# Optimization experiments

Hardware: AMD Instinct MI355X
Metric: run time of the kernel (lower is better)

Reference implementation:

```python
import math
import jax, jax.numpy as jnp
import numpy as np

B, S, D = 2, 2048, 1024
H = 16
R = 256
NC = 16
NE = 16
NK = 4096
KR = 256
TOPK = 8


def setup_inputs() -> dict:
    key = jax.random.key(0)
    ks = jax.random.split(key, 16)
    n = lambda k, shape, s: jax.random.normal(k, shape, jnp.float32) * s
    d = {}
    d['x'] = jax.random.normal(ks[0], (B, S, D), jnp.float32)
    d['importance'] = jax.random.uniform(ks[1], (B, S), jnp.float32)
    # global router weights (nn.Linear(d_model, n, bias=False) -> [n, d_model])
    d['Wc'] = n(ks[2], (NC, D), 0.02)
    d['WQ'] = n(ks[3], (NE, D), 0.02)
    d['WK'] = n(ks[4], (NE, D), 0.02)
    d['WV'] = n(ks[5], (NE, D), 0.02)
    d['Wm'] = n(ks[6], (NC, D), 0.02)
    # shared neuron pools (orthogonal init approximated by scaled gaussian)
    d['compress_neurons'] = n(ks[7], (NC, D, R), 1.0 / math.sqrt(D))
    d['expand_pool'] = n(ks[8], (NE, R, D), 1.0 / math.sqrt(R))
    d['knowledge_K'] = n(ks[9], (NK, KR), 0.02)
    d['knowledge_V'] = n(ks[10], (NK, D), 0.02)
    d['W_O'] = n(ks[11], (D, D), 1.0 / math.sqrt(D))
    d['g1'] = jnp.ones((D,), jnp.float32)
    d['b1'] = jnp.zeros((D,), jnp.float32)
    d['g2'] = jnp.ones((D,), jnp.float32)
    d['b2'] = jnp.zeros((D,), jnp.float32)
    return d


def _ln(x, g, b):
    mu = x.mean(-1, keepdims=True)
    v = ((x - mu) ** 2).mean(-1, keepdims=True)
    return (x - mu) * jax.lax.rsqrt(v + 1e-5) * g + b


def _route(nx, imp, W):
    # softmax over expert axis, importance-weighted pool over sequence, renormalize
    pref = jax.nn.softmax(nx @ W.T, axis=-1)          # [B,S,n]
    w = jnp.einsum('bs,bsn->bn', imp, pref)
    return w / (w.sum(-1, keepdims=True) + 1e-8)


def reference(x, importance, Wc, WQ, WK, WV, Wm, compress_neurons, expand_pool,
              knowledge_K, knowledge_V, W_O, g1, b1, g2, b2):
    Bx, Sx, Dm = x.shape
    dh = Dm // H
    # --- attention sub-block ---
    nx = _ln(x, g1, b1)
    cw = _route(nx, importance, Wc)
    qw = _route(nx, importance, WQ)
    kw = _route(nx, importance, WK)
    vw = _route(nx, importance, WV)
    sc = jnp.einsum('bn,ndr->bdr', cw, compress_neurons)   # per-batch compress [B,D,R]
    h = jnp.einsum('bsd,bdr->bsr', nx, sc)                 # [B,S,R]

    def expand(w):
        e = jnp.einsum('bn,nrd->brd', w, expand_pool)      # [B,R,D]
        return jnp.einsum('bsr,brd->bsd', h, e)            # [B,S,D]

    Q = expand(qw).reshape(Bx, Sx, H, dh).transpose(0, 2, 1, 3)
    K = expand(kw).reshape(Bx, Sx, H, dh).transpose(0, 2, 1, 3)
    V = expand(vw).reshape(Bx, Sx, H, dh).transpose(0, 2, 1, 3)
    scores = jnp.einsum('bhqd,bhkd->bhqk', Q, K) / math.sqrt(dh)
    causal = jnp.tril(jnp.ones((Sx, Sx), bool))
    scores = jnp.where(causal, scores, -jnp.inf)
    attn = jax.nn.softmax(scores, axis=-1)
    ao = jnp.einsum('bhqk,bhkd->bhqd', attn, V)
    ao = ao.transpose(0, 2, 1, 3).reshape(Bx, Sx, Dm)
    x = x + ao @ W_O.T
    # --- memory sub-block ---
    nx2 = _ln(x, g2, b2)
    mw = _route(nx2, importance, Wm)
    mc = jnp.einsum('bn,ndr->bdr', mw, compress_neurons)
    Qm = jnp.einsum('bsd,bdr->bsr', nx2, mc)              # [B,S,R]
    ms = Qm @ knowledge_K.T / math.sqrt(KR)               # [B,S,NK]
    tv, ti = jax.lax.top_k(ms, TOPK)                      # [B,S,k]
    w = jax.nn.softmax(tv, axis=-1)
    mem = jnp.einsum('bsk,bskd->bsd', w, knowledge_V[ti])
    return x + mem
```

## Files before the change

### kernel.cpp

```cpp
#include <hip/hip_runtime.h>
#include <hip/hip_bf16.h>
#include <math.h>

typedef __bf16 bf16;
typedef __attribute__((ext_vector_type(8))) __bf16 bf16x8;
typedef __attribute__((ext_vector_type(4))) __bf16 bf16x4;
typedef __attribute__((ext_vector_type(4))) float f32x4;
typedef __attribute__((ext_vector_type(16))) float f32x16;

#define EXP2N __builtin_amdgcn_exp2f

static __device__ __forceinline__ void gload_lds16(const bf16* g, bf16* l) {
  __builtin_amdgcn_global_load_lds((const __attribute__((address_space(1))) void*)g,
                                   (__attribute__((address_space(3))) void*)l, 16, 0, 0);
}

__global__ __launch_bounds__(256) void ln_kernel(
    const float* __restrict__ x, const float* __restrict__ gam, const float* __restrict__ bet,
    bf16* __restrict__ nxo)
{
  const int token = blockIdx.x;
  const int t = threadIdx.x, w = t >> 6, l = t & 63;
  __shared__ float red1[4], red2[4];
  float4 xv = ((const float4*)(x + (size_t)token * 1024))[t];
  float s  = xv.x + xv.y + xv.z + xv.w;
  float sq = xv.x*xv.x + xv.y*xv.y + xv.z*xv.z + xv.w*xv.w;
  #pragma unroll
  for (int off = 32; off > 0; off >>= 1) { s += __shfl_xor(s, off); sq += __shfl_xor(sq, off); }
  if (l == 0) { red1[w] = s; red2[w] = sq; }
  __syncthreads();
  s  = red1[0] + red1[1] + red1[2] + red1[3];
  sq = red2[0] + red2[1] + red2[2] + red2[3];
  const float mu  = s * (1.f / 1024.f);
  const float var = sq * (1.f / 1024.f) - mu * mu;
  const float rs  = rsqrtf(var + 1e-5f);
  float4 gv = ((const float4*)gam)[t];
  float4 bv = ((const float4*)bet)[t];
  bf16x4 pk = {(bf16)((xv.x - mu) * rs * gv.x + bv.x),
               (bf16)((xv.y - mu) * rs * gv.y + bv.y),
               (bf16)((xv.z - mu) * rs * gv.z + bv.z),
               (bf16)((xv.w - mu) * rs * gv.w + bv.w)};
  *(bf16x4*)(nxo + (size_t)token * 1024 + t * 4) = pk;
}

__global__ __launch_bounds__(256) void route_pool_kernel(
    const float* __restrict__ logits, const float* __restrict__ imp,
    float* __restrict__ racc, int ng, int gbase)
{
  const int w = threadIdx.x >> 6, l = threadIdx.x & 63;
  const int token = blockIdx.x * 4 + w;
  const int b = token >> 11;
  const int g = l >> 4, e = l & 15;
  if (g < ng) {
    float v = logits[(size_t)token * 128 + g * 16 + e];
    float mx = v;
    #pragma unroll
    for (int off = 1; off < 16; off <<= 1) mx = fmaxf(mx, __shfl_xor(mx, off));
    float ex = __expf(v - mx);
    float sm = ex;
    #pragma unroll
    for (int off = 1; off < 16; off <<= 1) sm += __shfl_xor(sm, off);
    atomicAdd(racc + ((((size_t)(token & 31)) * 5 + gbase + g) * 2 + b) * 16 + e,
              imp[token] * (ex / sm));
  }
}

__global__ __launch_bounds__(256) void mixA_kernel(
    const float* __restrict__ comp, const float* __restrict__ expd,
    const float* __restrict__ racc, bf16* __restrict__ sct, bf16* __restrict__ eqt)
{
  const int xb = blockIdx.x, sel = blockIdx.y, b = blockIdx.z;
  const int t = threadIdx.x;
  __shared__ float tile[64][65];
  __shared__ float psh[3][16];
  __shared__ float dsh[3];
  if (sel == 0) {
    if (t < 16) {
      float s = 0.f;
      for (int sl = 0; sl < 32; ++sl) s += racc[(((size_t)sl * 5 + 0) * 2 + b) * 16 + t];
      psh[0][t] = s;
    }
  } else {
    if (t < 48) {
      const int g = t >> 4, e = t & 15;
      float s = 0.f;
      for (int sl = 0; sl < 32; ++sl) s += racc[(((size_t)sl * 5 + 1 + g) * 2 + b) * 16 + e];
      psh[g][e] = s;
    }
  }
  __syncthreads();
  if (t < ((sel == 0) ? 1 : 3)) {
    float den = 1e-8f;
    #pragma unroll
    for (int e = 0; e < 16; ++e) den += psh[t][e];
    dsh[t] = 1.0f / den;
  }
  __syncthreads();

  const int ri = t >> 2, cc = (t & 3) << 4;
  if (sel == 0) {
    const int i0 = (xb & 15) * 64, j0 = (xb >> 4) * 64;
    const float inv = dsh[0];
    float acc[16];
    #pragma unroll
    for (int k = 0; k < 16; ++k) acc[k] = 0.f;
    const float* src0 = comp + ((size_t)(i0 + ri)) * 256 + j0 + cc;
    #pragma unroll 4
    for (int n = 0; n < 16; ++n) {
      const float wv = psh[0][n] * inv;
      const float4* sp = (const float4*)(src0 + (size_t)n * 262144);
      #pragma unroll
      for (int q = 0; q < 4; ++q) {
        float4 v = sp[q];
        acc[q*4+0] += wv * v.x; acc[q*4+1] += wv * v.y;
        acc[q*4+2] += wv * v.z; acc[q*4+3] += wv * v.w;
      }
    }
    #pragma unroll
    for (int k = 0; k < 16; ++k) tile[ri][cc + k] = acc[k];
    __syncthreads();
    union { bf16 h[16]; bf16x8 v[2]; } ob;
    #pragma unroll
    for (int k = 0; k < 16; ++k) ob.h[k] = (bf16)tile[cc + k][ri];
    bf16* dst = sct + ((size_t)b * 256 + j0 + ri) * 1024 + i0 + cc;
    ((bf16x8*)dst)[0] = ob.v[0];
    ((bf16x8*)dst)[1] = ob.v[1];
  } else {
    const int i0 = (xb & 3) * 64, j0 = (xb >> 2) * 64;
    const float inv0 = dsh[0], inv1 = dsh[1], inv2 = dsh[2];
    float acc[3][16];
    #pragma unroll
    for (int g = 0; g < 3; ++g)
      #pragma unroll
      for (int k = 0; k < 16; ++k) acc[g][k] = 0.f;
    const float* src0 = expd + ((size_t)(i0 + ri)) * 1024 + j0 + cc;
    #pragma unroll 2
    for (int n = 0; n < 16; ++n) {
      const float w0 = psh[0][n] * inv0;
      const float w1 = psh[1][n] * inv1;
      const float w2 = psh[2][n] * inv2;
      const float4* sp = (const float4*)(src0 + (size_t)n * 262144);
      #pragma unroll
      for (int q = 0; q < 4; ++q) {
        float4 v = sp[q];
        acc[0][q*4+0] += w0 * v.x; acc[0][q*4+1] += w0 * v.y;
        acc[0][q*4+2] += w0 * v.z; acc[0][q*4+3] += w0 * v.w;
        acc[1][q*4+0] += w1 * v.x; acc[1][q*4+1] += w1 * v.y;
        acc[1][q*4+2] += w1 * v.z; acc[1][q*4+3] += w1 * v.w;
        acc[2][q*4+0] += w2 * v.x; acc[2][q*4+1] += w2 * v.y;
        acc[2][q*4+2] += w2 * v.z; acc[2][q*4+3] += w2 * v.w;
      }
    }
    #pragma unroll 1
    for (int g = 0; g < 3; ++g) {
      __syncthreads();
      #pragma unroll
      for (int k = 0; k < 16; ++k) tile[ri][cc + k] = acc[g][k];
      __syncthreads();
      union { bf16 h[16]; bf16x8 v[2]; } ob;
      #pragma unroll
      for (int k = 0; k < 16; ++k) ob.h[k] = (bf16)tile[cc + k][ri];
      bf16* dst = eqt + (size_t)g * 524288 + ((size_t)b * 1024 + j0 + ri) * 256 + i0 + cc;
      ((bf16x8*)dst)[0] = ob.v[0];
      ((bf16x8*)dst)[1] = ob.v[1];
    }
  }
}

__global__ __launch_bounds__(256) void mixB_kernel(
    const float* __restrict__ comp, const float* __restrict__ racc,
    bf16* __restrict__ out)
{
  const int xb = blockIdx.x, b = blockIdx.z;
  const int t = threadIdx.x;
  __shared__ float tile[64][65];
  __shared__ float psh[16];
  __shared__ float dsh1;
  if (t < 16) {
    float s = 0.f;
    for (int sl = 0; sl < 32; ++sl) s += racc[(((size_t)sl * 5 + 4) * 2 + b) * 16 + t];
    psh[t] = s;
  }
  __syncthreads();
  if (t == 0) {
    float den = 1e-8f;
    #pragma unroll
    for (int e = 0; e < 16; ++e) den += psh[e];
    dsh1 = 1.0f / den;
  }
  __syncthreads();
  const int ri = t >> 2, cc = (t & 3) << 4;
  const int i0 = (xb & 15) * 64, j0 = (xb >> 4) * 64;
  const float inv = dsh1;
  float acc[16];
  #pragma unroll
  for (int k = 0; k < 16; ++k) acc[k] = 0.f;
  const float* src0 = comp + ((size_t)(i0 + ri)) * 256 + j0 + cc;
  #pragma unroll 4
  for (int n = 0; n < 16; ++n) {
    const float wv = psh[n] * inv;
    const float4* sp = (const float4*)(src0 + (size_t)n * 262144);
    #pragma unroll
    for (int q = 0; q < 4; ++q) {
      float4 v = sp[q];
      acc[q*4+0] += wv * v.x; acc[q*4+1] += wv * v.y;
      acc[q*4+2] += wv * v.z; acc[q*4+3] += wv * v.w;
    }
  }
  #pragma unroll
  for (int k = 0; k < 16; ++k) tile[ri][cc + k] = acc[k];
  __syncthreads();
  union { bf16 h[16]; bf16x8 v[2]; } ob;
  #pragma unroll
  for (int k = 0; k < 16; ++k) ob.h[k] = (bf16)tile[cc + k][ri];
  bf16* dst = out + ((size_t)b * 256 + j0 + ri) * 1024 + i0 + cc;
  ((bf16x8*)dst)[0] = ob.v[0];
  ((bf16x8*)dst)[1] = ob.v[1];
}

__global__ void cvt_bf16_kernel(const float* __restrict__ in, bf16* __restrict__ out, int n4)
{
  const int i = blockIdx.x * 256 + threadIdx.x;
  if (i < n4) {
    float4 v = ((const float4*)in)[i];
    bf16x4 o = {(bf16)v.x, (bf16)v.y, (bf16)v.z, (bf16)v.w};
    ((bf16x4*)out)[i] = o;
  }
}

__global__ void cvt_all_kernel(
    const float* __restrict__ w0, const float* __restrict__ w1,
    const float* __restrict__ w2, const float* __restrict__ w3,
    const float* __restrict__ w4, bf16* __restrict__ wcat,
    const float* __restrict__ wo, bf16* __restrict__ woo,
    const float* __restrict__ kk, bf16* __restrict__ kko)
{
  int i = blockIdx.x * 256 + threadIdx.x;
  if (i < 32768) {
    const int seg = i >> 12;
    bf16x4 o;
    if (seg < 5) {
      const float* src = (seg == 0) ? w0 : (seg == 1) ? w1 : (seg == 2) ? w2
                       : (seg == 3) ? w3 : w4;
      float4 v = ((const float4*)src)[i & 4095];
      o = (bf16x4){(bf16)v.x, (bf16)v.y, (bf16)v.z, (bf16)v.w};
    } else {
      o = (bf16x4){(bf16)0.f, (bf16)0.f, (bf16)0.f, (bf16)0.f};
    }
    ((bf16x4*)wcat)[i] = o;
  } else {
    i -= 32768;
    if (i < 262144) {
      float4 v = ((const float4*)wo)[i];
      ((bf16x4*)woo)[i] = (bf16x4){(bf16)v.x, (bf16)v.y, (bf16)v.z, (bf16)v.w};
    } else {
      i -= 262144;
      float4 v = ((const float4*)kk)[i];
      ((bf16x4*)kko)[i] = (bf16x4){(bf16)v.x, (bf16)v.y, (bf16)v.z, (bf16)v.w};
    }
  }
}

template<int CMODE>
__global__ __launch_bounds__(512) void gemm_bt(
    const bf16* __restrict__ A, const bf16* __restrict__ Bt, void* __restrict__ Cp,
    const float* __restrict__ resid, int M, int N, int K, int lda, int ldb,
    long sA, long sB, long sC, float scale)
{
  __shared__ alignas(16) bf16 As[2][128 * 32];
  __shared__ alignas(16) bf16 Bs[2][128 * 32];
  const int t = threadIdx.x, w = t >> 6, l = t & 63;
  const int llo = l & 15, lhi = l >> 4;
  const int wm = w >> 2, wn = w & 3;
  const int m0 = blockIdx.y * 128, n0 = blockIdx.x * 128;
  const int z = blockIdx.z;
  const bf16* Ab;
  const bf16* Bb;
  if (CMODE == 5) {
    Ab = A  + (size_t)(z >> 1) * sA + (size_t)(z & 1) * K;
    Bb = Bt + (size_t)(z >> 1) * sB + (size_t)(z & 1) * K;
  } else if (CMODE == 6) {
    Ab = A  + (size_t)(z & 1) * sA;
    Bb = Bt + (size_t)(z >> 1) * 524288 + (size_t)(z & 1) * sB;
  } else {
    Ab = A  + (size_t)z * sA;
    Bb = Bt + (size_t)z * sB;
  }
  f32x4 acc[4][2];
  #pragma unroll
  for (int i = 0; i < 4; ++i)
    #pragma unroll
    for (int j = 0; j < 2; ++j) acc[i][j] = (f32x4){0.f, 0.f, 0.f, 0.f};

  const int arow = t >> 2, akb = t & 3;
  const int akbs = akb ^ ((arow >> 1) & 3);
  const bf16* asrc = Ab + (size_t)(m0 + arow) * lda + akbs * 8;
  const bf16* bsrc = Bb + (size_t)(n0 + arow) * ldb + akbs * 8;
  bf16* adst0 = &As[0][t * 8];
  bf16* bdst0 = &Bs[0][t * 8];
  bf16* adst1 = &As[1][t * 8];
  bf16* bdst1 = &Bs[1][t * 8];

  gload_lds16(asrc, adst0);
  gload_lds16(bsrc, bdst0);

  int buf = 0;
  for (int kt = 0; kt < K; kt += 32) {
    __syncthreads();
    if (kt + 32 < K) {
      gload_lds16(asrc + kt + 32, buf ? adst0 : adst1);
      gload_lds16(bsrc + kt + 32, buf ? bdst0 : bdst1);
    }
    const bf16* Asb = As[buf];
    const bf16* Bsb = Bs[buf];
    bf16x8 af[4], bfr[2];
    #pragma unroll
    for (int fi = 0; fi < 4; ++fi) {
      int r = wm * 64 + fi * 16 + llo;
      af[fi] = *(const bf16x8*)((const char*)Asb + (r * 64 + ((lhi * 16) ^ (((r >> 1) & 3) << 4))));
    }
    #pragma unroll
    for (int fj = 0; fj < 2; ++fj) {
      int c = wn * 32 + fj * 16 + llo;
      bfr[fj] = *(const bf16x8*)((const char*)Bsb + (c * 64 + ((lhi * 16) ^ (((c >> 1) & 3) << 4))));
    }
    #pragma unroll
    for (int fi = 0; fi < 4; ++fi)
      #pragma unroll
      for (int fj = 0; fj < 2; ++fj)
        acc[fi][fj] = __builtin_amdgcn_mfma_f32_16x16x32_bf16(af[fi], bfr[fj], acc[fi][fj], 0, 0, 0);
    buf ^= 1;
  }

  size_t cbase;
  if (CMODE == 4) cbase = 0;
  else if (CMODE == 5) cbase = (size_t)(z >> 1) * sC;
  else if (CMODE == 6) cbase = (size_t)(z & 1) * sC;
  else cbase = (size_t)z * sC;

  #pragma unroll
  for (int fi = 0; fi < 4; ++fi)
    #pragma unroll
    for (int fj = 0; fj < 2; ++fj)
      #pragma unroll
      for (int jj = 0; jj < 4; ++jj) {
        int r = m0 + wm * 64 + fi * 16 + lhi * 4 + jj;
        int c = n0 + wn * 32 + fj * 16 + llo;
        size_t idx = cbase + (size_t)r * N + c;
        float v = acc[fi][fj][jj] * ((CMODE == 6) ? 1.0f : scale);
        if (CMODE == 0) {
          ((bf16*)Cp)[idx] = (bf16)v;
        } else if (CMODE == 3) {
          size_t idx3 = (((size_t)z * 16 + (c >> 6)) * 2048 + r) * 64 + (c & 63);
          ((bf16*)Cp)[idx3] = (bf16)v;
        } else if (CMODE == 4 || CMODE == 5) {
          atomicAdd(&((float*)Cp)[idx], v);
        } else if (CMODE == 6) {
          if ((z >> 1) == 0) {
            ((bf16*)Cp)[idx] = (bf16)v;
          } else {
            size_t idx3 = (((size_t)(z & 1) * 16 + (c >> 6)) * 2048 + r) * 64 + (c & 63);
            ((bf16*)resid)[idx3] = (bf16)(v * scale);
          }
        } else {
          if (CMODE == 2) v += resid[idx];
          ((float*)Cp)[idx] = v;
        }
      }
}

static __device__ __forceinline__ unsigned pk2f(float a, float b) {
  union { bf16 h[2]; unsigned u; } x;
  x.h[0] = (bf16)a; x.h[1] = (bf16)b; return x.u;
}

__global__ __launch_bounds__(512, 2) void attn7_kernel(
    const bf16* __restrict__ Qg, const bf16* __restrict__ Khg,
    const bf16* __restrict__ Vtg, bf16* __restrict__ aog)
{
  __shared__ alignas(16) bf16 KS[2][2][4096];
  __shared__ alignas(16) bf16 VS[2][2][4096];
  const int lin = blockIdx.x;
  const int hb = lin & 31, jj = (lin >> 5) & 7, phase = lin >> 8;
  const int h = hb >> 1, b = hb & 1;
  const int t = threadIdx.x, w = t >> 6, l = t & 63;
  const int half = w >> 2, wsub = w & 3;
  const int qi = l & 31, hi = l >> 5;
  const bf16* Qb = Qg  + ((size_t)b * 2048) * 1024 + h * 64;
  const bf16* Kh = Khg + ((size_t)(b * 16 + h)) * 2048 * 64;
  const bf16* Vh = Vtg + ((size_t)b * 1024 + h * 64) * 2048;
  bf16* Ob = aog + ((size_t)b * 2048) * 1024 + h * 64;

  float* PO = (float*)&KS[0][0][0];
  float* MM = (float*)((char*)&KS[0][0][0] + 40960);
  float* LL = MM + 128;

  auto ISSUE = [&](int bi, int kv0) {
    bf16* ksb = &KS[half][bi][0];
    bf16* vsb = &VS[half][bi][0];
    #pragma unroll
    for (int i = 0; i < 2; ++i) {
      int c = wsub * 128 + i * 64 + l;
      int row = c >> 3;
      int scol = (c & 7) ^ (row & 7);
      gload_lds16(Kh + (size_t)(kv0 + row) * 64 + scol * 8,
                  (bf16*)((char*)ksb + wsub * 2048 + i * 1024));
    }
    #pragma unroll
    for (int i = 0; i < 2; ++i) {
      int c = wsub * 128 + i * 64 + l;
      int row = c >> 3;
      int scol = (c & 7) ^ (row & 7);
      gload_lds16(Vh + (size_t)row * 2048 + kv0 + scol * 8,
                  (bf16*)((char*)vsb + wsub * 2048 + i * 1024));
    }
  };

  const int T = phase ? (15 - jj) : jj;
  const int q0 = T * 128 + wsub * 32;
  const int base_g = half * (T + 1);

  bf16x8 qf[4];
  #pragma unroll
  for (int dc = 0; dc < 4; ++dc)
    qf[dc] = *(const bf16x8*)(Qb + (size_t)(q0 + qi) * 1024 + dc * 16 + hi * 8);

  f32x16 o0, o1;
  #pragma unroll
  for (int r = 0; r < 16; ++r) { o0[r] = 0.f; o1[r] = 0.f; }
  float m_run = -INFINITY, l_run = 0.f;

  ISSUE(0, base_g * 64);

  auto STEP64 = [&](int bi, int s0) {
    const bool h2 = (s0 + 32 <= q0);
    bf16x8 kf[8];
    const bf16* ksb = &KS[half][bi][0];
    const bf16* vsb = &VS[half][bi][0];
    const int kr1 = qi, kr2 = 32 + qi;
    #pragma unroll
    for (int dc = 0; dc < 4; ++dc) {
      kf[dc]     = *(const bf16x8*)((const char*)ksb + kr1 * 128 +
                                    (((dc * 2 + hi) ^ (kr1 & 7)) << 4));
      kf[4 + dc] = *(const bf16x8*)((const char*)ksb + kr2 * 128 +
                                    (((dc * 2 + hi) ^ (kr2 & 7)) << 4));
    }
    f32x16 sv1, sv2;
    #pragma unroll
    for (int r = 0; r < 16; ++r) { sv1[r] = 0.f; sv2[r] = 0.f; }
    __builtin_amdgcn_s_setprio(1);
    #pragma unroll
    for (int dc = 0; dc < 4; ++dc)
      sv1 = __builtin_amdgcn_mfma_f32_32x32x16_bf16(kf[dc], qf[dc], sv1, 0, 0, 0);
    if (h2) {
      #pragma unroll
      for (int dc = 0; dc < 4; ++dc)
        sv2 = __builtin_amdgcn_mfma_f32_32x32x16_bf16(kf[4 + dc], qf[dc], sv2, 0, 0, 0);
    }
    __builtin_amdgcn_s_setprio(0);
    const int qe = qi - 4 * hi;
    if (s0 == q0) {
      #pragma unroll
      for (int r = 0; r < 16; ++r) {
        const int kvc = (r & 3) + 8 * (r >> 2);
        sv1[r] = (kvc > qe) ? -INFINITY : sv1[r];
      }
    }
    if (h2 && s0 + 32 == q0) {
      #pragma unroll
      for (int r = 0; r < 16; ++r) {
        const int kvc = (r & 3) + 8 * (r >> 2);
        sv2[r] = (kvc > qe) ? -INFINITY : sv2[r];
      }
    }
    float mx[8];
    #pragma unroll
    for (int i = 0; i < 8; ++i) mx[i] = fmaxf(sv1[2 * i], sv1[2 * i + 1]);
    if (h2) {
      #pragma unroll
      for (int i = 0; i < 8; ++i) mx[i] = fmaxf(mx[i], fmaxf(sv2[2 * i], sv2[2 * i + 1]));
    }
    #pragma unroll
    for (int i = 0; i < 4; ++i) mx[i] = fmaxf(mx[i], mx[i + 4]);
    float tm = fmaxf(fmaxf(mx[0], mx[1]), fmaxf(mx[2], mx[3]));
    tm = fmaxf(tm, __shfl_xor(tm, 32));
    if (!__all(tm <= m_run + 11.0f)) {
      const float mn = fmaxf(m_run, tm);
      const float alpha = EXP2N(m_run - mn);
      m_run = mn;
      l_run *= alpha;
      o0 *= alpha; o1 *= alpha;
    }
    float rs = 0.f;
    unsigned pk[16], ot[16];
    #pragma unroll
    for (int i = 0; i < 8; ++i) {
      float pa = EXP2N(sv1[2 * i]     - m_run);
      float pb = EXP2N(sv1[2 * i + 1] - m_run);
      rs += pa + pb;
      pk[i] = pk2f(pa, pb);
    }
    if (h2) {
      #pragma unroll
      for (int i = 0; i < 8; ++i) {
        float pa = EXP2N(sv2[2 * i]     - m_run);
        float pb = EXP2N(sv2[2 * i + 1] - m_run);
        rs += pa + pb;
        pk[8 + i] = pk2f(pa, pb);
      }
    }
    rs += __shfl_xor(rs, 32);
    l_run += rs;
    #pragma unroll
    for (int i = 0; i < 8; ++i) ot[i] = __shfl_xor(pk[i], 32);
    if (h2) {
      #pragma unroll
      for (int i = 0; i < 8; ++i) ot[8 + i] = __shfl_xor(pk[8 + i], 32);
    }
    __builtin_amdgcn_s_setprio(1);
    #pragma unroll
    for (int c2 = 0; c2 < 4; ++c2) {
      if (c2 < 2 || h2) {
        union { unsigned u[4]; bf16x8 v; } pf;
        pf.u[0] = hi ? ot[4 * c2 + 2] : pk[4 * c2 + 0];
        pf.u[1] = hi ? ot[4 * c2 + 3] : pk[4 * c2 + 1];
        pf.u[2] = hi ? pk[4 * c2 + 2] : ot[4 * c2 + 0];
        pf.u[3] = hi ? pk[4 * c2 + 3] : ot[4 * c2 + 1];
        const int d0 = qi, d1 = 32 + qi;
        bf16x8 v0 = *(const bf16x8*)((const char*)vsb + d0 * 128 +
                                     (((c2 * 2 + hi) ^ (d0 & 7)) << 4));
        bf16x8 v1 = *(const bf16x8*)((const char*)vsb + d1 * 128 +
                                     (((c2 * 2 + hi) ^ (d1 & 7)) << 4));
        o0 = __builtin_amdgcn_mfma_f32_32x32x16_bf16(v0, pf.v, o0, 0, 0, 0);
        o1 = __builtin_amdgcn_mfma_f32_32x32x16_bf16(v1, pf.v, o1, 0, 0, 0);
      }
    }
    __builtin_amdgcn_s_setprio(0);
  };

  #pragma unroll 1
  for (int st = 0; st <= T; ++st) {
    const int bi = st & 1;
    if (st < T) {
      ISSUE(bi ^ 1, (base_g + st + 1) * 64);
      asm volatile("s_waitcnt vmcnt(4)" ::: "memory");
    } else {
      asm volatile("s_waitcnt vmcnt(0)" ::: "memory");
    }
    __builtin_amdgcn_s_barrier();
    const int s0 = (base_g + st) * 64;
    if (s0 <= q0) STEP64(bi, s0);
    __builtin_amdgcn_s_barrier();
  }

  if (half == 1) {
    #pragma unroll
    for (int r = 0; r < 16; ++r) {
      const int d0 = (r & 3) + 8 * (r >> 2) + 4 * hi;
      PO[(wsub * 32 + qi) * 65 + d0]      = o0[r];
      PO[(wsub * 32 + qi) * 65 + 32 + d0] = o1[r];
    }
    if (hi == 0) { MM[wsub * 32 + qi] = m_run; LL[wsub * 32 + qi] = l_run; }
  }
  __syncthreads();
  if (half == 0) {
    const float m1 = MM[wsub * 32 + qi], l1 = LL[wsub * 32 + qi];
    const float m = fmaxf(m_run, m1);
    const float a0 = EXP2N(m_run - m), a1 = EXP2N(m1 - m);
    const float inv = 1.0f / (a0 * l_run + a1 * l1);
    #pragma unroll
    for (int rg = 0; rg < 4; ++rg) {
      union { bf16 h4[4]; unsigned long long u; } pr0, pr1;
      #pragma unroll
      for (int e = 0; e < 4; ++e) {
        const int r = rg * 4 + e;
        const int d0 = (r & 3) + 8 * (r >> 2) + 4 * hi;
        pr0.h4[e] = (bf16)((a0 * o0[r] + a1 * PO[(wsub * 32 + qi) * 65 + d0])      * inv);
        pr1.h4[e] = (bf16)((a0 * o1[r] + a1 * PO[(wsub * 32 + qi) * 65 + 32 + d0]) * inv);
      }
      *(unsigned long long*)(Ob + (size_t)(q0 + qi) * 1024 +  0 + rg * 8 + hi * 4) = pr0.u;
      *(unsigned long long*)(Ob + (size_t)(q0 + qi) * 1024 + 32 + rg * 8 + hi * 4) = pr1.u;
    }
  }
}

static __device__ __forceinline__ void ce_desc(float& a, float& b) {
  float hi = fmaxf(a, b), lo = fminf(a, b); a = hi; b = lo;
}
static __device__ __forceinline__ void merge8(float r[8], const float o[8]) {
  float c[8];
  #pragma unroll
  for (int i = 0; i < 8; ++i) c[i] = fmaxf(r[i], o[7 - i]);
  ce_desc(c[0], c[4]); ce_desc(c[1], c[5]); ce_desc(c[2], c[6]); ce_desc(c[3], c[7]);
  ce_desc(c[0], c[2]); ce_desc(c[1], c[3]); ce_desc(c[4], c[6]); ce_desc(c[5], c[7]);
  ce_desc(c[0], c[1]); ce_desc(c[2], c[3]); ce_desc(c[4], c[5]); ce_desc(c[6], c[7]);
  #pragma unroll
  for (int i = 0; i < 8; ++i) r[i] = c[i];
}
static __device__ __forceinline__ unsigned long long fkey(float v, int idx) {
  unsigned u = __float_as_uint(v);
  u = (u & 0x80000000u) ? ~u : (u | 0x80000000u);
  return ((unsigned long long)u << 32) | (unsigned)(0xFFFFFFFFu - (unsigned)idx);
}

__global__ __launch_bounds__(256) void topk3_kernel(
    const bf16* __restrict__ ms, const float* __restrict__ kV, float* __restrict__ outp)
{
  const int token = blockIdx.x;
  const int t = threadIdx.x, w = t >> 6, l = t & 63;
  __shared__ unsigned long long cand[4096];
  __shared__ float wmax[32];
  __shared__ float wv[8];
  __shared__ int   wi[8];
  __shared__ int   cnt;
  if (t == 0) cnt = 0;

  const bf16* mrow = ms + (size_t)token * 4096;
  float vv[16];
  #pragma unroll
  for (int c = 0; c < 2; ++c) {
    bf16x8 rv = ((const bf16x8*)mrow)[t + c * 256];
    #pragma unroll
    for (int j = 0; j < 8; ++j) vv[c * 8 + j] = (float)rv[j];
  }

  float m = vv[0];
  #pragma unroll
  for (int j = 1; j < 16; ++j) m = fmaxf(m, vv[j]);

  float r[8];
  r[0] = m;
  #pragma unroll
  for (int i = 1; i < 8; ++i) r[i] = -INFINITY;
  #pragma unroll
  for (int st = 0; st < 6; ++st) {
    const int off = 1 << st;
    float o[8];
    #pragma unroll
    for (int i = 0; i < 8; ++i) o[i] = __shfl_xor(r[i], off);
    merge8(r, o);
  }
  if (l == 0) {
    #pragma unroll
    for (int i = 0; i < 8; ++i) wmax[w * 8 + i] = r[i];
  }
  __syncthreads();

  float a[8], bb[8];
  #pragma unroll
  for (int i = 0; i < 8; ++i) { a[i] = wmax[i]; bb[i] = wmax[8 + i]; }
  merge8(a, bb);
  #pragma unroll
  for (int i = 0; i < 8; ++i) bb[i] = wmax[16 + i];
  {
    float c2[8];
    #pragma unroll
    for (int i = 0; i < 8; ++i) c2[i] = wmax[24 + i];
    merge8(bb, c2);
  }
  merge8(a, bb);
  const float t8 = a[7];

  #pragma unroll
  for (int c = 0; c < 2; ++c) {
    const int base = (t + c * 256) * 8;
    #pragma unroll
    for (int j = 0; j < 8; ++j) {
      float v = vv[c * 8 + j];
      if (v >= t8) { int pos = atomicAdd(&cnt, 1); cand[pos] = fkey(v, base + j); }
    }
  }
  __syncthreads();

  if (w == 0) {
    const int n = cnt;
    unsigned long long prev = ~0ULL;
    float vk[8]; int ik[8];
    #pragma unroll
    for (int k = 0; k < 8; ++k) {
      unsigned long long best = 0;
      for (int i = l; i < n; i += 64) {
        unsigned long long c = cand[i];
        if (c < prev && c > best) best = c;
      }
      #pragma unroll
      for (int st = 0; st < 6; ++st) {
        const int off = 1 << st;
        unsigned bh = (unsigned)(best >> 32), bl = (unsigned)best;
        unsigned oh = __shfl_xor(bh, off), ol = __shfl_xor(bl, off);
        unsigned long long ob = ((unsigned long long)oh << 32) | ol;
        if (ob > best) best = ob;
      }
      prev = best;
      unsigned u = (unsigned)(best >> 32);
      u = (u & 0x80000000u) ? (u ^ 0x80000000u) : ~u;
      vk[k] = __uint_as_float(u);
      ik[k] = (int)(0xFFFFFFFFu - (unsigned)(best & 0xFFFFFFFFu));
    }
    if (l == 0) {
      const float mx = vk[0];
      float den = 0.f, ex[8];
      #pragma unroll
      for (int k = 0; k < 8; ++k) { ex[k] = __expf(vk[k] - mx); den += ex[k]; }
      const float inv = 1.0f / den;
      #pragma unroll
      for (int k = 0; k < 8; ++k) { wv[k] = ex[k] * inv; wi[k] = ik[k]; }
    }
  }
  __syncthreads();

  float a0 = 0, a1 = 0, a2 = 0, a3 = 0;
  #pragma unroll
  for (int k = 0; k < 8; ++k) {
    const float wk = wv[k];
    float4 vr = *(const float4*)(kV + (size_t)wi[k] * 1024 + t * 4);
    a0 += wk * vr.x; a1 += wk * vr.y; a2 += wk * vr.z; a3 += wk * vr.w;
  }
  float4* op = (float4*)(outp + (size_t)token * 1024) + t;
  float4 cur = *op;
  cur.x += a0; cur.y += a1; cur.z += a2; cur.w += a3;
  *op = cur;
}

extern "C" void kernel_launch(void* const* d_in, const int* in_sizes, int n_in,
                              void* d_out, int out_size, void* d_ws, size_t ws_size,
                              hipStream_t stream)
{
  (void)in_sizes; (void)n_in; (void)out_size; (void)ws_size;
  const float* x    = (const float*)d_in[0];
  const float* imp  = (const float*)d_in[1];
  const float* Wc   = (const float*)d_in[2];
  const float* WQ   = (const float*)d_in[3];
  const float* WK   = (const float*)d_in[4];
  const float* WV   = (const float*)d_in[5];
  const float* Wm   = (const float*)d_in[6];
  const float* comp = (const float*)d_in[7];
  const float* expd = (const float*)d_in[8];
  const float* kK   = (const float*)d_in[9];
  const float* kV   = (const float*)d_in[10];
  const float* WO   = (const float*)d_in[11];
  const float* g1   = (const float*)d_in[12];
  const float* b1   = (const float*)d_in[13];
  const float* g2   = (const float*)d_in[14];
  const float* b2   = (const float*)d_in[15];
  float* out = (float*)d_out;
  char* ws = (char*)d_ws;
  const size_t MB = 1u << 20;
  float* racc    = (float*)(ws);
  float* logits1 = (float*)(ws + 64 * 1024);
  float* logits2 = (float*)(ws + 64 * 1024 + 2 * MB);
  float* accf1   = (float*)(ws + 64 * 1024 + 4 * MB);
  float* accf2   = (float*)(ws + 64 * 1024 + 8 * MB);
  bf16*  Wcatb   = (bf16*)(ws + 13 * MB);
  char* ar = ws + 14 * MB;
  bf16* nx   = (bf16*)(ar);
  bf16* sct  = (bf16*)(ar +  8 * MB);
  bf16* eqt  = (bf16*)(ar +  9 * MB);
  bf16* evt  = (bf16*)(ar + 11 * MB);
  bf16* hb   = (bf16*)(ar + 12 * MB);
  bf16* Qb   = (bf16*)(ar + 14 * MB);
  bf16* Kb   = (bf16*)(ar + 22 * MB);
  bf16* Vtb  = (bf16*)(ar + 30 * MB);
  bf16* aob  = (bf16*)(ar + 38 * MB);
  bf16* WOb  = (bf16*)(ar + 46 * MB);
  bf16* nx2  = (bf16*)(ar);
  bf16* mct  = (bf16*)(ar +  8 * MB);
  bf16* Qmb  = (bf16*)(ar +  9 * MB);
  bf16* kKb  = (bf16*)(ar + 11 * MB);
  bf16* msb  = (bf16*)(ar + 13 * MB);

  hipMemsetAsync(ws, 0, 12 * MB + 65536, stream);
  cvt_all_kernel<<<2176, 256, 0, stream>>>(Wc, WQ, WK, WV, Wm, Wcatb, WO, WOb, kK, kKb);

  ln_kernel<<<4096, 256, 0, stream>>>(x, g1, b1, nx);
  gemm_bt<4><<<dim3(1, 32, 4), 512, 0, stream>>>(nx, Wcatb, logits1, nullptr,
        4096, 128, 256, 1024, 1024, 256L, 256L, 0L, 1.0f);
  route_pool_kernel<<<1024, 256, 0, stream>>>(logits1, imp, racc, 4, 0);
  mixA_kernel<<<dim3(64, 2, 2), 256, 0, stream>>>(comp, expd, racc, sct, eqt);
  gemm_bt<5><<<dim3(2, 16, 4), 512, 0, stream>>>(nx, sct, accf1, nullptr, 2048, 256, 512,
        1024, 1024, (long)2048 * 1024, (long)256 * 1024, (long)2048 * 256, 1.0f);
  cvt_bf16_kernel<<<1024, 256, 0, stream>>>(accf1, hb, 262144);
  gemm_bt<6><<<dim3(8, 16, 4), 512, 0, stream>>>(hb, eqt, Qb, (const float*)Kb,
        2048, 1024, 256, 256, 256,
        (long)2048 * 256, (long)1024 * 256, (long)2048 * 1024, 0.18033688f);
  gemm_bt<0><<<dim3(16, 8, 2), 512, 0, stream>>>(evt, hb, Vtb, nullptr, 1024, 2048, 256,
        256, 256, (long)1024 * 256, (long)2048 * 256, (long)1024 * 2048, 1.0f);
  attn7_kernel<<<512, 512, 0, stream>>>(Qb, Kb, Vtb, aob);
  gemm_bt<2><<<dim3(8, 32, 1), 512, 0, stream>>>(aob, WOb, out, x, 4096, 1024, 1024,
        1024, 1024, 0L, 0L, 0L, 1.0f);
  ln_kernel<<<4096, 256, 0, stream>>>(out, g2, b2, nx2);
  gemm_bt<4><<<dim3(1, 32, 4), 512, 0, stream>>>(nx2, Wcatb + 64 * 1024, logits2, nullptr,
        4096, 128, 256, 1024, 1024, 256L, 256L, 0L, 1.0f);
  route_pool_kernel<<<1024, 256, 0, stream>>>(logits2, imp, racc, 1, 4);
  mixB_kernel<<<dim3(64, 1, 2), 256, 0, stream>>>(comp, racc, mct);
  gemm_bt<5><<<dim3(2, 16, 4), 512, 0, stream>>>(nx2, mct, accf2, nullptr, 2048, 256, 512,
        1024, 1024, (long)2048 * 1024, (long)256 * 1024, (long)2048 * 256, 1.0f);
  cvt_bf16_kernel<<<1024, 256, 0, stream>>>(accf2, Qmb, 262144);
  gemm_bt<0><<<dim3(32, 16, 2), 512, 0, stream>>>(Qmb, kKb, msb, nullptr, 2048, 4096, 256,
        256, 256, (long)2048 * 256, 0L, (long)2048 * 4096, 0.0625f);
  topk3_kernel<<<4096, 256, 0, stream>>>(msb, kV, out);
}
```

Baseline: 244.3 us.

## Deepen GEMM LDS pipeline to four buffers with explicit vmcnt waits

```diff
diff --git a/kernel.cpp b/kernel.cpp
--- a/kernel.cpp
+++ b/kernel.cpp
@@ -267,8 +267,8 @@
     const float* __restrict__ resid, int M, int N, int K, int lda, int ldb,
     long sA, long sB, long sC, float scale)
 {
-  __shared__ alignas(16) bf16 As[2][128 * 32];
-  __shared__ alignas(16) bf16 Bs[2][128 * 32];
+  __shared__ alignas(16) bf16 As[4][4096];
+  __shared__ alignas(16) bf16 Bs[4][4096];
   const int t = threadIdx.x, w = t >> 6, l = t & 63;
   const int llo = l & 15, lhi = l >> 4;
   const int wm = w >> 2, wn = w & 3;
@@ -296,23 +296,28 @@
   const int akbs = akb ^ ((arow >> 1) & 3);
   const bf16* asrc = Ab + (size_t)(m0 + arow) * lda + akbs * 8;
   const bf16* bsrc = Bb + (size_t)(n0 + arow) * ldb + akbs * 8;
-  bf16* adst0 = &As[0][t * 8];
-  bf16* bdst0 = &Bs[0][t * 8];
-  bf16* adst1 = &As[1][t * 8];
-  bf16* bdst1 = &Bs[1][t * 8];
-
-  gload_lds16(asrc, adst0);
-  gload_lds16(bsrc, bdst0);
-
-  int buf = 0;
-  for (int kt = 0; kt < K; kt += 32) {
-    __syncthreads();
-    if (kt + 32 < K) {
-      gload_lds16(asrc + kt + 32, buf ? adst0 : adst1);
-      gload_lds16(bsrc + kt + 32, buf ? bdst0 : bdst1);
-    }
-    const bf16* Asb = As[buf];
-    const bf16* Bsb = Bs[buf];
+
+  gload_lds16(asrc,      &As[0][t * 8]);
+  gload_lds16(bsrc,      &Bs[0][t * 8]);
+  gload_lds16(asrc + 32, &As[1][t * 8]);
+  gload_lds16(bsrc + 32, &Bs[1][t * 8]);
+
+  const int nt = K >> 5;
+  for (int it = 0; it < nt; ++it) {
+    const int kt = it << 5;
+    if (it + 2 < nt) {
+      const int nb = (it + 2) & 3;
+      gload_lds16(asrc + kt + 64, &As[nb][t * 8]);
+      gload_lds16(bsrc + kt + 64, &Bs[nb][t * 8]);
+      asm volatile("s_waitcnt vmcnt(4)" ::: "memory");
+    } else if (it + 1 < nt) {
+      asm volatile("s_waitcnt vmcnt(2)" ::: "memory");
+    } else {
+      asm volatile("s_waitcnt vmcnt(0)" ::: "memory");
+    }
+    __builtin_amdgcn_s_barrier();
+    const bf16* Asb = As[it & 3];
+    const bf16* Bsb = Bs[it & 3];
     bf16x8 af[4], bfr[2];
     #pragma unroll
     for (int fi = 0; fi < 4; ++fi) {
@@ -329,7 +334,6 @@
       #pragma unroll
       for (int fj = 0; fj < 2; ++fj)
         acc[fi][fj] = __builtin_amdgcn_mfma_f32_16x16x32_bf16(af[fi], bfr[fj], acc[fi][fj], 0, 0, 0);
-    buf ^= 1;
   }
 
   size_t cbase;
```

After: 246.9 us. No clear change (+1.0%).
